# Optimization experiments

Hardware: AMD Instinct MI355X
Metric: run time of the kernel (lower is better)

## Reference

```python
import jax, jax.numpy as jnp
import numpy as np

N0, N1, N2 = 100000, 40000, 10000
E1, E2 = 640000, 160000
D_IN, D_HID, D_OUT = 256, 256, 128


def segment_mean(msgs, dst, num_segments):
    # PyG mean aggregation: sum of incoming messages / count, 0 for isolated nodes
    s = jax.ops.segment_sum(msgs, dst, num_segments=num_segments)
    cnt = jax.ops.segment_sum(jnp.ones((msgs.shape[0],), msgs.dtype), dst,
                              num_segments=num_segments)
    return s / jnp.maximum(cnt, 1.0)[:, None]


def setup_inputs() -> dict:
    key = jax.random.key(0)
    ks = jax.random.split(key, 10)
    x = jax.random.normal(ks[0], (N0, D_IN), jnp.float32)
    W1l = jax.random.normal(ks[1], (D_IN, D_HID), jnp.float32) * 0.05
    b1 = jnp.zeros((D_HID,), jnp.float32)
    W1r = jax.random.normal(ks[2], (D_IN, D_HID), jnp.float32) * 0.05
    W2l = jax.random.normal(ks[3], (D_HID, D_OUT), jnp.float32) * 0.05
    b2 = jnp.zeros((D_OUT,), jnp.float32)
    W2r = jax.random.normal(ks[4], (D_HID, D_OUT), jnp.float32) * 0.05
    src1 = jax.random.randint(ks[5], (E1,), 0, N0)
    dst1 = jax.random.randint(ks[6], (E1,), 0, N1)
    src2 = jax.random.randint(ks[7], (E2,), 0, N1)
    dst2 = jax.random.randint(ks[8], (E2,), 0, N2)
    return {"x": x, "W1l": W1l, "b1": b1, "W1r": W1r,
            "W2l": W2l, "b2": b2, "W2r": W2r,
            "src1": src1, "dst1": dst1, "src2": src2, "dst2": dst2}


def reference(x, W1l, b1, W1r, W2l, b2, W2r, src1, dst1, src2, dst2):
    # Layer 1: SAGEConv(D_IN -> D_HID) on bipartite (x, x[:N1]) + ReLU
    x_t1 = x[:N1]
    aggr1 = segment_mean(x[src1], dst1, N1)          # [N1, D_IN]
    h = aggr1 @ W1l + b1 + x_t1 @ W1r                # lin_l(aggr)+bias + lin_r(root)
    h = jax.nn.relu(h)
    # Layer 2: SAGEConv(D_HID -> D_OUT) on bipartite (h, h[:N2]) + sigmoid
    x_t2 = h[:N2]
    aggr2 = segment_mean(h[src2], dst2, N2)          # [N2, D_HID]
    out = aggr2 @ W2l + b2 + x_t2 @ W2r
    return jax.nn.sigmoid(out)                       # [N2, D_OUT]
```

## Files before the change

kernel.cpp:

```cpp
#include <hip/hip_runtime.h>
#include <math.h>

#define N0_C  100000
#define N1_C  40000
#define N2_C  10000
#define E1_C  640000
#define E2_C  160000
#define D_IN_C  256
#define D_HID_C 256
#define D_OUT_C 128

#define MAXDEG 128

typedef __attribute__((ext_vector_type(8))) short short8;
typedef __attribute__((ext_vector_type(4))) float float4v;

__device__ __forceinline__ unsigned short f2bf(float f) {
    unsigned int u = __float_as_uint(f);
    return (unsigned short)((u + 0x7FFFu + ((u >> 16) & 1u)) >> 16);
}
__device__ __forceinline__ float bf2f(unsigned int h) {
    return __uint_as_float(h << 16);
}

#define PREP_CONV  6400000
#define PREP_TW    196608
#define PREP_TOTAL (PREP_CONV + PREP_TW + N1_C + N2_C)

__global__ void prep_kernel(const float* __restrict__ x,
                            const float* __restrict__ W1l,
                            const float* __restrict__ W1r,
                            const float* __restrict__ W2l,
                            const float* __restrict__ W2r,
                            unsigned short* __restrict__ xb,
                            unsigned short* __restrict__ wt1l,
                            unsigned short* __restrict__ wt1r,
                            unsigned short* __restrict__ wt2l,
                            unsigned short* __restrict__ wt2r,
                            int* __restrict__ cnt) {
    int stride = gridDim.x * blockDim.x;
    for (int id = blockIdx.x * blockDim.x + threadIdx.x; id < PREP_TOTAL; id += stride) {
        if (id < PREP_CONV) {
            float4 v = ((const float4*)x)[id];
            unsigned long long u = (unsigned long long)f2bf(v.x)
                                 | ((unsigned long long)f2bf(v.y) << 16)
                                 | ((unsigned long long)f2bf(v.z) << 32)
                                 | ((unsigned long long)f2bf(v.w) << 48);
            ((unsigned long long*)xb)[id] = u;
        } else if (id < PREP_CONV + PREP_TW) {
            int t = id - PREP_CONV;
            const float* W; unsigned short* Wt; int N; int off;
            if (t < 65536)       { W = W1l; Wt = wt1l; N = 256; off = t; }
            else if (t < 131072) { W = W1r; Wt = wt1r; N = 256; off = t - 65536; }
            else if (t < 163840) { W = W2l; Wt = wt2l; N = 128; off = t - 131072; }
            else                 { W = W2r; Wt = wt2r; N = 128; off = t - 163840; }
            int k = off / N, n = off - k * N;
            Wt[n * 256 + k] = f2bf(W[off]);
        } else {
            cnt[id - PREP_CONV - PREP_TW] = 0;
        }
    }
}

__global__ void scatter_idx_kernel(const int* __restrict__ src1,
                                   const int* __restrict__ dst1,
                                   const int* __restrict__ src2,
                                   const int* __restrict__ dst2,
                                   int* __restrict__ cnt1, int* __restrict__ cnt2,
                                   int* __restrict__ perm2D1,
                                   int* __restrict__ perm2D2) {
    int e = blockIdx.x * blockDim.x + threadIdx.x;
    if (e < E1_C) {
        int d = min(max(dst1[e], 0), N1_C - 1);
        int pos = atomicAdd(&cnt1[d], 1);
        if (pos < MAXDEG) perm2D1[d * MAXDEG + pos] = src1[e];
    } else if (e < E1_C + E2_C) {
        int e2 = e - E1_C;
        int d = min(max(dst2[e2], 0), N2_C - 1);
        int pos = atomicAdd(&cnt2[d], 1);
        if (pos < MAXDEG) perm2D2[d * MAXDEG + pos] = src2[e2];
    }
}

__global__ __launch_bounds__(256)
void gather_mean_bf16_kernel(const unsigned short* __restrict__ feat,
                             const int* __restrict__ cnt,
                             const int* __restrict__ perm2D,
                             unsigned short* __restrict__ aggr,
                             int n, int nfeat) {
    int node = blockIdx.x * 4 + (threadIdx.x >> 6);
    int lane = threadIdx.x & 63;
    if (node >= n) return;
    const int half = lane >> 5;
    const int lc   = lane & 31;
    const int c_true = cnt[node];
    const int m = min(max(c_true, 0), MAXDEG);
    const int* __restrict__ row = perm2D + (size_t)node * MAXDEG;

    float a[8];
    #pragma unroll
    for (int j = 0; j < 8; ++j) a[j] = 0.f;

    int i = 0;
    for (; i + 8 <= m; i += 8) {
        int s0 = min(max(row[i     + half], 0), nfeat - 1);
        int s1 = min(max(row[i + 2 + half], 0), nfeat - 1);
        int s2 = min(max(row[i + 4 + half], 0), nfeat - 1);
        int s3 = min(max(row[i + 6 + half], 0), nfeat - 1);
        short8 v0 = *(const short8*)(feat + (size_t)s0 * 256 + lc * 8);
        short8 v1 = *(const short8*)(feat + (size_t)s1 * 256 + lc * 8);
        short8 v2 = *(const short8*)(feat + (size_t)s2 * 256 + lc * 8);
        short8 v3 = *(const short8*)(feat + (size_t)s3 * 256 + lc * 8);
        #pragma unroll
        for (int j = 0; j < 8; ++j)
            a[j] += (bf2f((unsigned int)(unsigned short)v0[j])
                   + bf2f((unsigned int)(unsigned short)v1[j]))
                  + (bf2f((unsigned int)(unsigned short)v2[j])
                   + bf2f((unsigned int)(unsigned short)v3[j]));
    }
    for (; i + 2 <= m; i += 2) {
        int s = min(max(row[i + half], 0), nfeat - 1);
        short8 v = *(const short8*)(feat + (size_t)s * 256 + lc * 8);
        #pragma unroll
        for (int j = 0; j < 8; ++j)
            a[j] += bf2f((unsigned int)(unsigned short)v[j]);
    }
    if (i < m && half == 0) {
        int s = min(max(row[i], 0), nfeat - 1);
        short8 v = *(const short8*)(feat + (size_t)s * 256 + lc * 8);
        #pragma unroll
        for (int j = 0; j < 8; ++j)
            a[j] += bf2f((unsigned int)(unsigned short)v[j]);
    }

    #pragma unroll
    for (int j = 0; j < 8; ++j) a[j] += __shfl_xor(a[j], 32, 64);

    if (half == 0) {
        float inv = (c_true > 0) ? 1.0f / (float)c_true : 0.0f;
        short8 o;
        #pragma unroll
        for (int j = 0; j < 8; ++j) o[j] = (short)f2bf(a[j] * inv);
        *(short8*)(aggr + (size_t)node * 256 + lc * 8) = o;
    }
}

__global__ __launch_bounds__(512)
void mfma_gemm1_kernel(const unsigned short* A0,
                       const unsigned short* A1,
                       const unsigned short* __restrict__ Wt0,
                       const unsigned short* __restrict__ Wt1,
                       const float* __restrict__ bias,
                       unsigned short* out_bf,
                       int M) {
    __shared__ unsigned short As[64][72];
    __shared__ unsigned short Bs[256][72];

    const int tid  = threadIdx.x;
    const int lane = tid & 63;
    const int wid  = tid >> 6;
    const int wm   = wid & 1;
    const int wn   = wid >> 1;
    const int lr   = lane & 15;
    const int kq   = lane >> 4;
    const int row0 = blockIdx.x * 64;

    float4v acc[2][4];
    #pragma unroll
    for (int a = 0; a < 2; ++a)
        #pragma unroll
        for (int b = 0; b < 4; ++b)
            #pragma unroll
            for (int c = 0; c < 4; ++c) acc[a][b][c] = 0.f;

    for (int p = 0; p < 2; ++p) {
        const unsigned short* A  = p ? A1  : A0;
        const unsigned short* __restrict__ Wt = p ? Wt1 : Wt0;
        for (int kt = 0; kt < 4; ++kt) {
            const int k0 = kt * 64;
            __syncthreads();
            {
                int r = tid >> 3, sc = (tid & 7) * 8;
                int row = row0 + r;
                if (row > M - 1) row = M - 1;
                *(short8*)&As[r][sc] = *(const short8*)(A + (size_t)row * 256 + k0 + sc);
            }
            #pragma unroll
            for (int i = 0; i < 4; ++i) {
                int idx = tid + i * 512;
                int r = idx >> 3, sc = (idx & 7) * 8;
                *(short8*)&Bs[r][sc] = *(const short8*)(Wt + (size_t)r * 256 + k0 + sc);
            }
            __syncthreads();
            #pragma unroll
            for (int ks = 0; ks < 64; ks += 32) {
                short8 af[2], bfr[4];
                #pragma unroll
                for (int t = 0; t < 2; ++t)
                    af[t]  = *(const short8*)&As[wm * 32 + t * 16 + lr][ks + kq * 8];
                #pragma unroll
                for (int t = 0; t < 4; ++t)
                    bfr[t] = *(const short8*)&Bs[wn * 64 + t * 16 + lr][ks + kq * 8];
                #pragma unroll
                for (int ar = 0; ar < 2; ++ar)
                    #pragma unroll
                    for (int bc = 0; bc < 4; ++bc)
                        acc[ar][bc] = __builtin_amdgcn_mfma_f32_16x16x32_bf16(
                            af[ar], bfr[bc], acc[ar][bc], 0, 0, 0);
            }
        }
    }

    #pragma unroll
    for (int bc = 0; bc < 4; ++bc) {
        int col = wn * 64 + bc * 16 + lr;
        float bv = bias[col];
        #pragma unroll
        for (int ar = 0; ar < 2; ++ar) {
            int rowb = row0 + wm * 32 + ar * 16 + kq * 4;
            #pragma unroll
            for (int i = 0; i < 4; ++i) {
                int row = rowb + i;
                if (row < M)
                    out_bf[(size_t)row * 256 + col] = f2bf(fmaxf(acc[ar][bc][i] + bv, 0.f));
            }
        }
    }
}

__global__ __launch_bounds__(256)
void mfma_gemm2_kernel(const unsigned short* __restrict__ A0,
                       const unsigned short* __restrict__ A1,
                       const unsigned short* __restrict__ Wt0,
                       const unsigned short* __restrict__ Wt1,
                       const float* __restrict__ bias,
                       float* __restrict__ out_f,
                       int M, int N) {
    __shared__ unsigned short As[64][72];
    __shared__ unsigned short Bs[128][72];

    const int tid  = threadIdx.x;
    const int lane = tid & 63;
    const int wid  = tid >> 6;
    const int wm   = wid & 1;
    const int wn   = wid >> 1;
    const int lr   = lane & 15;
    const int kq   = lane >> 4;
    const int row0 = blockIdx.x * 64;

    float4v acc[2][4];
    #pragma unroll
    for (int a = 0; a < 2; ++a)
        #pragma unroll
        for (int b = 0; b < 4; ++b)
            #pragma unroll
            for (int c = 0; c < 4; ++c) acc[a][b][c] = 0.f;

    for (int p = 0; p < 2; ++p) {
        const unsigned short* __restrict__ A  = p ? A1  : A0;
        const unsigned short* __restrict__ Wt = p ? Wt1 : Wt0;
        for (int kt = 0; kt < 4; ++kt) {
            const int k0 = kt * 64;
            __syncthreads();
            #pragma unroll
            for (int i = 0; i < 2; ++i) {
                int idx = tid + i * 256;
                int r = idx >> 3, sc = (idx & 7) * 8;
                int row = row0 + r;
                if (row > M - 1) row = M - 1;
                *(short8*)&As[r][sc] = *(const short8*)(A + (size_t)row * 256 + k0 + sc);
            }
            #pragma unroll
            for (int i = 0; i < 4; ++i) {
                int idx = tid + i * 256;
                int r = idx >> 3, sc = (idx & 7) * 8;
                *(short8*)&Bs[r][sc] = *(const short8*)(Wt + (size_t)r * 256 + k0 + sc);
            }
            __syncthreads();
            #pragma unroll
            for (int ks = 0; ks < 64; ks += 32) {
                short8 af[2], bfr[4];
                #pragma unroll
                for (int t = 0; t < 2; ++t)
                    af[t]  = *(const short8*)&As[wm * 32 + t * 16 + lr][ks + kq * 8];
                #pragma unroll
                for (int t = 0; t < 4; ++t)
                    bfr[t] = *(const short8*)&Bs[wn * 64 + t * 16 + lr][ks + kq * 8];
                #pragma unroll
                for (int ar = 0; ar < 2; ++ar)
                    #pragma unroll
                    for (int bc = 0; bc < 4; ++bc)
                        acc[ar][bc] = __builtin_amdgcn_mfma_f32_16x16x32_bf16(
                            af[ar], bfr[bc], acc[ar][bc], 0, 0, 0);
            }
        }
    }

    #pragma unroll
    for (int bc = 0; bc < 4; ++bc) {
        int col = wn * 64 + bc * 16 + lr;
        float bv = bias[col];
        #pragma unroll
        for (int ar = 0; ar < 2; ++ar) {
            int rowb = row0 + wm * 32 + ar * 16 + kq * 4;
            #pragma unroll
            for (int i = 0; i < 4; ++i) {
                int row = rowb + i;
                if (row < M)
                    out_f[(size_t)row * N + col] =
                        1.0f / (1.0f + __expf(-(acc[ar][bc][i] + bv)));
            }
        }
    }
}

extern "C" void kernel_launch(void* const* d_in, const int* in_sizes, int n_in,
                              void* d_out, int out_size, void* d_ws, size_t ws_size,
                              hipStream_t stream) {
    const float* x   = (const float*)d_in[0];
    const float* W1l = (const float*)d_in[1];
    const float* b1  = (const float*)d_in[2];
    const float* W1r = (const float*)d_in[3];
    const float* W2l = (const float*)d_in[4];
    const float* b2  = (const float*)d_in[5];
    const float* W2r = (const float*)d_in[6];
    const int* src1  = (const int*)d_in[7];
    const int* dst1  = (const int*)d_in[8];
    const int* src2  = (const int*)d_in[9];
    const int* dst2  = (const int*)d_in[10];
    float* out = (float*)d_out;

    unsigned short* us = (unsigned short*)d_ws;
    unsigned short* xb    = us;                          us += (size_t)N0_C * 256;
    unsigned short* h     = xb;
    unsigned short* aggr1 = us;                          us += (size_t)N1_C * 256;
    unsigned short* aggr2 = aggr1;
    unsigned short* wt1l  = us;                          us += 256 * 256;
    unsigned short* wt1r  = us;                          us += 256 * 256;
    unsigned short* wt2l  = us;                          us += 128 * 256;
    unsigned short* wt2r  = us;                          us += 128 * 256;
    int* ip = (int*)us;
    int* cnt1    = ip;                 ip += N1_C;
    int* cnt2    = ip;                 ip += N2_C;
    int* perm2D1 = ip;                 ip += (size_t)N1_C * MAXDEG;
    int* perm2D2 = ip;                 ip += (size_t)N2_C * MAXDEG;

    prep_kernel<<<2048, 256, 0, stream>>>(x, W1l, W1r, W2l, W2r,
                                          xb, wt1l, wt1r, wt2l, wt2r, cnt1);

    scatter_idx_kernel<<<(E1_C + E2_C + 255) / 256, 256, 0, stream>>>(
        src1, dst1, src2, dst2, cnt1, cnt2, perm2D1, perm2D2);

    gather_mean_bf16_kernel<<<(N1_C + 3) / 4, 256, 0, stream>>>(xb, cnt1, perm2D1,
                                                                aggr1, N1_C, N0_C);
    mfma_gemm1_kernel<<<(N1_C + 63) / 64, 512, 0, stream>>>(aggr1, xb, wt1l, wt1r,
                                                            b1, h, N1_C);

    gather_mean_bf16_kernel<<<(N2_C + 3) / 4, 256, 0, stream>>>(h, cnt2, perm2D2,
                                                                aggr2, N2_C, N1_C);
    mfma_gemm2_kernel<<<(N2_C + 63) / 64, 256, 0, stream>>>(aggr2, h, wt2l, wt2r,
                                                            b2, out, N2_C, D_OUT_C);
}
```

Measured before the change: 334.3 us.

## Fuse edge scatter into prep and use swizzled direct-to-LDS loads in GEMM1

The edge-bucketing scatter moves into the prep kernel, and counter zeroing becomes a hipMemsetAsync, so one kernel launch disappears. Layer-1 weights are pre-transposed into an XOR-swizzled tile layout. GEMM1 then loads A and B tiles with global_load_lds (direct global-to-LDS) into unpadded swizzled shared memory, reading fragments with the matching XOR pattern. This is meant to cut register staging, LDS footprint and bank conflicts, at the cost of adding a memset call and a tightly coupled layout.

```diff
diff --git a/kernel.cpp b/kernel.cpp
--- a/kernel.cpp
+++ b/kernel.cpp
@@ -23,21 +23,34 @@
     return __uint_as_float(h << 16);
 }
 
+__device__ __forceinline__ void gload_lds16(const void* g, void* l) {
+    __builtin_amdgcn_global_load_lds(
+        (const __attribute__((address_space(1))) unsigned int*)g,
+        (__attribute__((address_space(3))) unsigned int*)l, 16, 0, 0);
+}
+
 #define PREP_CONV  6400000
 #define PREP_TW    196608
-#define PREP_TOTAL (PREP_CONV + PREP_TW + N1_C + N2_C)
+#define PREP_E     (E1_C + E2_C)
+#define PREP_TOTAL (PREP_CONV + PREP_TW + PREP_E)
 
 __global__ void prep_kernel(const float* __restrict__ x,
                             const float* __restrict__ W1l,
                             const float* __restrict__ W1r,
                             const float* __restrict__ W2l,
                             const float* __restrict__ W2r,
+                            const int* __restrict__ src1,
+                            const int* __restrict__ dst1,
+                            const int* __restrict__ src2,
+                            const int* __restrict__ dst2,
                             unsigned short* __restrict__ xb,
                             unsigned short* __restrict__ wt1l,
                             unsigned short* __restrict__ wt1r,
                             unsigned short* __restrict__ wt2l,
                             unsigned short* __restrict__ wt2r,
-                            int* __restrict__ cnt) {
+                            int* __restrict__ cnt1, int* __restrict__ cnt2,
+                            int* __restrict__ perm2D1,
+                            int* __restrict__ perm2D2) {
     int stride = gridDim.x * blockDim.x;
     for (int id = blockIdx.x * blockDim.x + threadIdx.x; id < PREP_TOTAL; id += stride) {
         if (id < PREP_CONV) {
@@ -49,36 +62,36 @@
             ((unsigned long long*)xb)[id] = u;
         } else if (id < PREP_CONV + PREP_TW) {
             int t = id - PREP_CONV;
-            const float* W; unsigned short* Wt; int N; int off;
-            if (t < 65536)       { W = W1l; Wt = wt1l; N = 256; off = t; }
-            else if (t < 131072) { W = W1r; Wt = wt1r; N = 256; off = t - 65536; }
-            else if (t < 163840) { W = W2l; Wt = wt2l; N = 128; off = t - 131072; }
-            else                 { W = W2r; Wt = wt2r; N = 128; off = t - 163840; }
-            int k = off / N, n = off - k * N;
-            Wt[n * 256 + k] = f2bf(W[off]);
+            if (t < 131072) {
+                const float* W = (t < 65536) ? W1l : W1r;
+                unsigned short* Wt = (t < 65536) ? wt1l : wt1r;
+                int off = t & 65535;
+                int k = off >> 8, n = off & 255;
+                int c  = (k >> 3) & 7;
+                int cp = c ^ (n & 7);
+                int slot = (k >> 6) * 16384 + (n * 8 + cp) * 8 + (k & 7);
+                Wt[slot] = f2bf(W[off]);
+            } else {
+                int t2 = t - 131072;
+                const float* W = (t2 < 32768) ? W2l : W2r;
+                unsigned short* Wt = (t2 < 32768) ? wt2l : wt2r;
+                int off = t2 & 32767;
+                int k = off >> 7, n = off & 127;
+                Wt[n * 256 + k] = f2bf(W[off]);
+            }
         } else {
-            cnt[id - PREP_CONV - PREP_TW] = 0;
-        }
-    }
-}
-
-__global__ void scatter_idx_kernel(const int* __restrict__ src1,
-                                   const int* __restrict__ dst1,
-                                   const int* __restrict__ src2,
-                                   const int* __restrict__ dst2,
-                                   int* __restrict__ cnt1, int* __restrict__ cnt2,
-                                   int* __restrict__ perm2D1,
-                                   int* __restrict__ perm2D2) {
-    int e = blockIdx.x * blockDim.x + threadIdx.x;
-    if (e < E1_C) {
-        int d = min(max(dst1[e], 0), N1_C - 1);
-        int pos = atomicAdd(&cnt1[d], 1);
-        if (pos < MAXDEG) perm2D1[d * MAXDEG + pos] = src1[e];
-    } else if (e < E1_C + E2_C) {
-        int e2 = e - E1_C;
-        int d = min(max(dst2[e2], 0), N2_C - 1);
-        int pos = atomicAdd(&cnt2[d], 1);
-        if (pos < MAXDEG) perm2D2[d * MAXDEG + pos] = src2[e2];
+            int e = id - PREP_CONV - PREP_TW;
+            if (e < E1_C) {
+                int d = min(max(dst1[e], 0), N1_C - 1);
+                int pos = atomicAdd(&cnt1[d], 1);
+                if (pos < MAXDEG) perm2D1[d * MAXDEG + pos] = src1[e];
+            } else {
+                int e2 = e - E1_C;
+                int d = min(max(dst2[e2], 0), N2_C - 1);
+                int pos = atomicAdd(&cnt2[d], 1);
+                if (pos < MAXDEG) perm2D2[d * MAXDEG + pos] = src2[e2];
+            }
+        }
     }
 }
 
@@ -153,8 +166,8 @@
                        const float* __restrict__ bias,
                        unsigned short* out_bf,
                        int M) {
-    __shared__ unsigned short As[64][72];
-    __shared__ unsigned short Bs[256][72];
+    __shared__ unsigned short As[64 * 64];
+    __shared__ unsigned short Bs[256 * 64];
 
     const int tid  = threadIdx.x;
     const int lane = tid & 63;
@@ -165,6 +178,11 @@
     const int kq   = lane >> 4;
     const int row0 = blockIdx.x * 64;
 
+    const int a_r = wid * 8 + (lane >> 3);
+    const int a_c = (lane & 7) ^ (lane >> 3);
+    int a_row = row0 + a_r;
+    if (a_row > M - 1) a_row = M - 1;
+
     float4v acc[2][4];
     #pragma unroll
     for (int a = 0; a < 2; ++a)
@@ -179,28 +197,26 @@
         for (int kt = 0; kt < 4; ++kt) {
             const int k0 = kt * 64;
             __syncthreads();
-            {
-                int r = tid >> 3, sc = (tid & 7) * 8;
-                int row = row0 + r;
-                if (row > M - 1) row = M - 1;
-                *(short8*)&As[r][sc] = *(const short8*)(A + (size_t)row * 256 + k0 + sc);
-            }
-            #pragma unroll
-            for (int i = 0; i < 4; ++i) {
-                int idx = tid + i * 512;
-                int r = idx >> 3, sc = (idx & 7) * 8;
-                *(short8*)&Bs[r][sc] = *(const short8*)(Wt + (size_t)r * 256 + k0 + sc);
-            }
+            gload_lds16(A + (size_t)a_row * 256 + k0 + a_c * 8, &As[wid * 512]);
+            #pragma unroll
+            for (int i = 0; i < 4; ++i)
+                gload_lds16(Wt + (size_t)kt * 16384 + ((wid * 4 + i) * 64 + lane) * 8,
+                            &Bs[(wid * 4 + i) * 512]);
             __syncthreads();
             #pragma unroll
             for (int ks = 0; ks < 64; ks += 32) {
+                const int ch = kq + (ks >> 3);
                 short8 af[2], bfr[4];
                 #pragma unroll
-                for (int t = 0; t < 2; ++t)
-                    af[t]  = *(const short8*)&As[wm * 32 + t * 16 + lr][ks + kq * 8];
-                #pragma unroll
-                for (int t = 0; t < 4; ++t)
-                    bfr[t] = *(const short8*)&Bs[wn * 64 + t * 16 + lr][ks + kq * 8];
+                for (int t = 0; t < 2; ++t) {
+                    int r = wm * 32 + t * 16 + lr;
+                    af[t] = *(const short8*)&As[r * 64 + (ch ^ (lr & 7)) * 8];
+                }
+                #pragma unroll
+                for (int t = 0; t < 4; ++t) {
+                    int r = wn * 64 + t * 16 + lr;
+                    bfr[t] = *(const short8*)&Bs[r * 64 + (ch ^ (lr & 7)) * 8];
+                }
                 #pragma unroll
                 for (int ar = 0; ar < 2; ++ar)
                     #pragma unroll
@@ -345,11 +361,12 @@
     int* perm2D1 = ip;                 ip += (size_t)N1_C * MAXDEG;
     int* perm2D2 = ip;                 ip += (size_t)N2_C * MAXDEG;
 
+    hipMemsetAsync(cnt1, 0, (size_t)(N1_C + N2_C) * sizeof(int), stream);
+
     prep_kernel<<<2048, 256, 0, stream>>>(x, W1l, W1r, W2l, W2r,
-                                          xb, wt1l, wt1r, wt2l, wt2r, cnt1);
-
-    scatter_idx_kernel<<<(E1_C + E2_C + 255) / 256, 256, 0, stream>>>(
-        src1, dst1, src2, dst2, cnt1, cnt2, perm2D1, perm2D2);
+                                          src1, dst1, src2, dst2,
+                                          xb, wt1l, wt1r, wt2l, wt2r,
+                                          cnt1, cnt2, perm2D1, perm2D2);
 
     gather_mean_bf16_kernel<<<(N1_C + 3) / 4, 256, 0, stream>>>(xb, cnt1, perm2D1,
                                                                 aggr1, N1_C, N0_C);
```

Result: no change. 333.2 us (-0.3%).
